# Optimization experiments

Measured on AMD Instinct MI355X. Metric: run time of the kernel, lower is better.

Reference implementation:

```python
import jax, jax.numpy as jnp
import numpy as np

N_BANKS = 16
BAND = 4
D = 32          # n_neurons_per_hidd_bank
N_IN = 3072     # n_input_neurons
N_OUT = 1000    # n_output_neurons
B = 8192        # batch size
IDX_INPUT = [0, 1]
IDX_OUTPUT = [14, 15]
# edge list (source, target), target-major, ascending sources per target --
# matches the torch loop order (np.where over bank_conn[:, i_target])
EDGES = [(s, t) for t in range(N_BANKS) for s in range(max(0, t - BAND), t)]
E = len(EDGES)  # 54
TGT_EDGES = [[e for e, (s, t) in enumerate(EDGES) if t == tt] for tt in range(N_BANKS)]
BN_EPS = 1e-5


def _bn(a):
    # BatchNorm1d in training mode: batch mean, biased batch variance
    m = a.mean(axis=0)
    v = a.var(axis=0)
    return (a - m) * jax.lax.rsqrt(v + BN_EPS)


def setup_inputs() -> dict:
    key = jax.random.key(0)
    ks = jax.random.split(key, 8)
    return {
        "x": jax.random.normal(ks[0], (B, N_IN), jnp.float32),
        "bn_gamma": jnp.ones((N_IN,), jnp.float32),
        "bn_beta": jnp.zeros((N_IN,), jnp.float32),
        "W_in": jax.random.normal(ks[1], (len(IDX_INPUT), N_IN, D), jnp.float32) / np.float32(np.sqrt(N_IN)),
        "b_in": jax.random.normal(ks[2], (len(IDX_INPUT), D), jnp.float32) / np.float32(np.sqrt(N_IN)),
        "Wg": jax.random.normal(ks[3], (E, D), jnp.float32) / np.float32(np.sqrt(D)),
        "Wd": jax.random.normal(ks[4], (E, D, D), jnp.float32) / np.float32(np.sqrt(D)),
        "bd": jax.random.normal(ks[5], (E, D), jnp.float32) / np.float32(np.sqrt(D)),
        "Wout": jax.random.normal(ks[6], (len(IDX_OUTPUT), D, N_OUT), jnp.float32) / np.float32(np.sqrt(D)),
    }


def reference(x, bn_gamma, bn_beta, W_in, b_in, Wg, Wd, bd, Wout):
    # input batch norm (affine)
    x = _bn(x) * bn_gamma + bn_beta
    acts = [None] * N_BANKS
    for k, i in enumerate(IDX_INPUT):
        acts[i] = jax.nn.relu(x @ W_in[k] + b_in[k])  # [B, D]
    total_gate = jnp.zeros((x.shape[0], 1), x.dtype)
    for t in range(N_BANKS):
        acc = acts[t]  # non-None only for input banks
        for e in TGT_EDGES[t]:
            s = EDGES[e][0]
            gate = jnp.clip(acts[s] @ Wg[e], 0.0, 1.0)[:, None]  # hardtanh(.,0,1), [B,1]
            total_gate = total_gate + gate
            data = acts[s] @ Wd[e] + bd[e]                       # [B, D]
            acc = gate * data if acc is None else acc + gate * data
        acts[t] = _bn(jax.nn.relu(acc))  # hidden batch norm, affine=False
    output = None
    for k, i in enumerate(IDX_OUTPUT):
        d = acts[i] @ Wout[k]  # Linear(D, N_OUT, bias=False)
        output = d if output is None else output + d
    return output, total_gate
```

## Files before the change

### kernel.cpp

```cpp
#include <hip/hip_runtime.h>


#define BATCH 8192
#define NIN 3072
#define DD 32
#define NB 16
#define NOUT 1000
#define TGOFF (BATCH * NOUT)
#define BNEPS 1e-5f

#define O_SUM 0
#define O_SUM2 3072
#define O_STATS2 6144
#define O_TG 22528
#define ZERO_FLOATS 30720
#define O_SCALE 30720
#define O_SHIFT 33792
#define O_BIAS 36864
#define O_BP 36928
#define O_ACTS 233536
#define O_ACC (O_ACTS + 2 * BATCH * DD)

__global__ void __launch_bounds__(256) k_stats(const float* __restrict__ x, float* __restrict__ ws) {
    int c = blockIdx.x * 256 + threadIdx.x;
    const float* p = x + (size_t)blockIdx.y * 256 * NIN + c;
    float s = 0.f, s2 = 0.f;
#pragma unroll 8
    for (int i = 0; i < 256; i++) { float v = p[(size_t)i * NIN]; s += v; s2 += v * v; }
    atomicAdd(&ws[O_SUM + c], s);
    atomicAdd(&ws[O_SUM2 + c], s2);
}

__global__ void __launch_bounds__(256) k_prep(float* __restrict__ ws, const float* __restrict__ g,
                                              const float* __restrict__ b, const float* __restrict__ b_in) {
    int c = blockIdx.x * 256 + threadIdx.x;
    float mean = ws[O_SUM + c] * (1.f / BATCH);
    float var = ws[O_SUM2 + c] * (1.f / BATCH) - mean * mean;
    float sc = g[c] * rsqrtf(fmaxf(var, 0.f) + BNEPS);
    ws[O_SCALE + c] = sc;
    ws[O_SHIFT + c] = b[c] - mean * sc;
    if (c < 64) ws[O_BIAS + c] = b_in[c];
}

__global__ void __launch_bounds__(256) k_bias(float* __restrict__ ws, const float* __restrict__ W_in) {
    int bank = blockIdx.x & 1, jc = blockIdx.x >> 1;
    int d = threadIdx.x & 31, js = threadIdx.x >> 5;
    int j0 = jc * 256 + js * 32;
    float a = 0.f;
    for (int j = 0; j < 32; j++)
        a += ws[O_SHIFT + j0 + j] * W_in[(size_t)bank * NIN * DD + (size_t)(j0 + j) * DD + d];
    __shared__ float red[8][32];
    red[js][d] = a;
    __syncthreads();
    if (threadIdx.x < 32) {
        float t = 0.f;
#pragma unroll
        for (int g8 = 0; g8 < 8; g8++) t += red[g8][threadIdx.x];
        atomicAdd(&ws[O_BIAS + bank * 32 + threadIdx.x], t);
    }
}

__global__ void __launch_bounds__(256) k_bfold(float* __restrict__ ws, const float* __restrict__ W_in) {
    int idx = blockIdx.x * 256 + threadIdx.x;
    int j = idx >> 6, c = idx & 63;
    ws[O_BP + idx] = ws[O_SCALE + j] * W_in[(size_t)(c >> 5) * NIN * DD + (size_t)j * DD + (c & 31)];
}

__global__ void __launch_bounds__(256) k_gemm3(const float* __restrict__ x, float* __restrict__ ws) {
    __shared__ float xL[64][20];
    __shared__ float bL[16][64];
    int tid = threadIdx.x;
    int row0 = blockIdx.x * 64;
    int k00 = blockIdx.y * 768;
    const float* bp = ws + O_BP;
    float acc[4][4] = {};
    int tx = tid & 15, rt = tid >> 4;
    int lr = tid >> 2, lq = tid & 3;
    int br = tid >> 4, bq = tid & 15;
    for (int kc = 0; kc < 48; kc++) {
        int k0 = k00 + kc * 16;
        float4 xv = *(const float4*)&x[(size_t)(row0 + lr) * NIN + k0 + lq * 4];
        float4 bv = *(const float4*)&bp[(size_t)(k0 + br) * 64 + bq * 4];
        __syncthreads();
        *(float4*)&xL[lr][lq * 4] = xv;
        *(float4*)&bL[br][bq * 4] = bv;
        __syncthreads();
#pragma unroll
        for (int kk = 0; kk < 16; kk += 4) {
            float4 b0 = *(float4*)&bL[kk][tx * 4];
            float4 b1 = *(float4*)&bL[kk + 1][tx * 4];
            float4 b2 = *(float4*)&bL[kk + 2][tx * 4];
            float4 b3 = *(float4*)&bL[kk + 3][tx * 4];
#pragma unroll
            for (int j = 0; j < 4; j++) {
                float4 xv4 = *(float4*)&xL[rt * 4 + j][kk];
                acc[j][0] += xv4.x * b0.x + xv4.y * b1.x + xv4.z * b2.x + xv4.w * b3.x;
                acc[j][1] += xv4.x * b0.y + xv4.y * b1.y + xv4.z * b2.y + xv4.w * b3.y;
                acc[j][2] += xv4.x * b0.z + xv4.y * b1.z + xv4.z * b2.z + xv4.w * b3.z;
                acc[j][3] += xv4.x * b0.w + xv4.y * b1.w + xv4.z * b2.w + xv4.w * b3.w;
            }
        }
    }
    float* dst = ws + O_ACC + (size_t)blockIdx.y * (BATCH * 64);
#pragma unroll
    for (int j = 0; j < 4; j++) {
        float4 v = make_float4(acc[j][0], acc[j][1], acc[j][2], acc[j][3]);
        *(float4*)&dst[(size_t)(row0 + rt * 4 + j) * 64 + tx * 4] = v;
    }
}

__global__ void __launch_bounds__(256) k_act(float* __restrict__ ws) {
    int i4 = (blockIdx.x * 256 + threadIdx.x) * 4;
    const float* ac = ws + O_ACC;
    float4 s0 = *(const float4*)&ac[i4];
    float4 s1 = *(const float4*)&ac[524288 + i4];
    float4 s2 = *(const float4*)&ac[1048576 + i4];
    float4 s3 = *(const float4*)&ac[1572864 + i4];
    int c = i4 & 63, row = i4 >> 6;
    const float* bias = ws + O_BIAS;
    float4 v;
    v.x = fmaxf(s0.x + s1.x + s2.x + s3.x + bias[c], 0.f);
    v.y = fmaxf(s0.y + s1.y + s2.y + s3.y + bias[c + 1], 0.f);
    v.z = fmaxf(s0.z + s1.z + s2.z + s3.z + bias[c + 2], 0.f);
    v.w = fmaxf(s0.w + s1.w + s2.w + s3.w + bias[c + 3], 0.f);
    int bank = c >> 5, dd = c & 31;
    *(float4*)&ws[O_ACTS + ((size_t)bank * BATCH + row) * DD + dd] = v;
}

__global__ void __launch_bounds__(256) k_bank(int t, float* __restrict__ ws,
                                              const float* __restrict__ Wg, const float* __restrict__ Wd,
                                              const float* __restrict__ bd) {
    __shared__ float asrcL[4][8][32];
    __shared__ float WdL[4][1024];
    __shared__ float mML[4][32], ivL[4][32];
    __shared__ float red[8][64];
    int tid = threadIdx.x;
    int rg = tid >> 5, d = tid & 31;
    int row0 = blockIdx.x * 8;
    int slot = blockIdx.x & 15;
    float* acts = ws + O_ACTS;
    float* stats = ws + O_STATS2;
    int nE = t < 4 ? t : 4;
    int s0 = t - nE;
    int eb = (t <= 4) ? t * (t - 1) / 2 : 10 + 4 * (t - 5);
    for (int p = tid; p < nE * 256; p += 256)
        ((float4*)&WdL[0][0])[p] = ((const float4*)(Wd + (size_t)eb * 1024))[p];
    float wgr[4], bdr[4];
#pragma unroll
    for (int ei = 0; ei < 4; ei++) {
        wgr[ei] = (ei < nE) ? Wg[(eb + ei) * 32 + d] : 0.f;
        bdr[ei] = (ei < nE) ? bd[(eb + ei) * 32 + d] : 0.f;
    }
    if (tid < nE * 32) {
        int si = tid >> 5, dd = tid & 31;
        const float* st = stats + (size_t)(s0 + si) * 16 * 64;
        float sm = 0.f, sq = 0.f;
#pragma unroll
        for (int sl = 0; sl < 16; sl++) { sm += st[sl * 64 + dd]; sq += st[sl * 64 + 32 + dd]; }
        float m = sm * (1.f / BATCH);
        float var = sq * (1.f / BATCH) - m * m;
        mML[si][dd] = m;
        ivL[si][dd] = rsqrtf(fmaxf(var, 0.f) + BNEPS);
    }
    float cur = (t < 2) ? acts[((size_t)t * BATCH + row0 + rg) * DD + d] : 0.f;
    __syncthreads();
#pragma unroll 4
    for (int si = 0; si < nE; si++)
        asrcL[si][rg][d] = (acts[((size_t)(s0 + si) * BATCH + row0 + rg) * DD + d] - mML[si][d]) * ivL[si][d];
    __syncthreads();
    float tg = 0.f;
#pragma unroll
    for (int ei = 0; ei < 4; ei++) {
        if (ei < nE) {
            float g = asrcL[ei][rg][d] * wgr[ei];
            g += __shfl_xor(g, 1); g += __shfl_xor(g, 2); g += __shfl_xor(g, 4);
            g += __shfl_xor(g, 8); g += __shfl_xor(g, 16);
            g = fminf(fmaxf(g, 0.f), 1.f);
            tg += g;
            float dat = bdr[ei];
            const float* ar = asrcL[ei][rg];
            const float* wc = &WdL[ei][d];
#pragma unroll
            for (int k = 0; k < 32; k += 4) {
                float4 a4 = *(const float4*)&ar[k];
                dat += a4.x * wc[k * 32] + a4.y * wc[(k + 1) * 32]
                     + a4.z * wc[(k + 2) * 32] + a4.w * wc[(k + 3) * 32];
            }
            cur += g * dat;
        }
    }
    float v = fmaxf(cur, 0.f);
    acts[((size_t)t * BATCH + row0 + rg) * DD + d] = v;
    if (d == 0 && nE > 0) ws[O_TG + row0 + rg] += tg;
    red[rg][d] = v; red[rg][32 + d] = v * v;
    __syncthreads();
    if (tid < 64) {
        float a = 0.f;
#pragma unroll
        for (int g8 = 0; g8 < 8; g8++) a += red[g8][tid];
        atomicAdd(&stats[((size_t)t * 16 + slot) * 64 + tid], a);
    }
}

__global__ void __launch_bounds__(256) k_out(const float* __restrict__ ws, const float* __restrict__ Wout,
                                             float* __restrict__ out) {
    __shared__ float aLt[32][68];
    __shared__ float wL[32][128];
    __shared__ float mIv[2][2][32];
    int tid = threadIdx.x;
    int row0 = blockIdx.x * 64;
    int col0 = blockIdx.y * 128;
    const float* acts = ws + O_ACTS;
    if (blockIdx.y == 0 && tid < 64) out[TGOFF + row0 + tid] = ws[O_TG + row0 + tid];
    if (tid < 64) {
        int bi = tid >> 5, d = tid & 31;
        const float* st = ws + O_STATS2 + (size_t)(14 + bi) * 16 * 64;
        float sm = 0.f, sq = 0.f;
#pragma unroll
        for (int sl = 0; sl < 16; sl++) { sm += st[sl * 64 + d]; sq += st[sl * 64 + 32 + d]; }
        float m = sm * (1.f / BATCH);
        float var = sq * (1.f / BATCH) - m * m;
        mIv[bi][0][d] = m;
        mIv[bi][1][d] = rsqrtf(fmaxf(var, 0.f) + BNEPS);
    }
    int tx = tid & 31, ty = tid >> 5;
    int c4 = col0 + tx * 4;
    bool c4ok = (c4 + 3 < NOUT);
    float acc[8][4] = {};
    for (int bi = 0; bi < 2; bi++) {
        __syncthreads();
        {
            int d = tid & 31, r0 = tid >> 5;
            float m = mIv[bi][0][d], iv = mIv[bi][1][d];
            const float* ap = acts + ((size_t)(14 + bi) * BATCH + row0) * DD + d;
#pragma unroll
            for (int i = 0; i < 8; i++) {
                int r = r0 + 8 * i;
                aLt[d][r] = (ap[(size_t)r * DD] - m) * iv;
            }
        }
        {
            const float* wp = Wout + (size_t)bi * DD * NOUT + c4;
            int kk0 = tid >> 5;
#pragma unroll
            for (int i = 0; i < 4; i++) {
                int kk = kk0 + 8 * i;
                const float* wr = wp + (size_t)kk * NOUT;
                float4 v;
                if (c4ok) {
                    v = *(const float4*)wr;
                } else {
                    v.x = (c4 + 0 < NOUT) ? wr[0] : 0.f;
                    v.y = (c4 + 1 < NOUT) ? wr[1] : 0.f;
                    v.z = (c4 + 2 < NOUT) ? wr[2] : 0.f;
                    v.w = (c4 + 3 < NOUT) ? wr[3] : 0.f;
                }
                *(float4*)&wL[kk][tx * 4] = v;
            }
        }
        __syncthreads();
#pragma unroll 4
        for (int k = 0; k < 32; k++) {
            float4 w = *(float4*)&wL[k][tx * 4];
            float4 a0 = *(float4*)&aLt[k][ty * 8];
            float4 a1 = *(float4*)&aLt[k][ty * 8 + 4];
            float ar[8] = {a0.x, a0.y, a0.z, a0.w, a1.x, a1.y, a1.z, a1.w};
            float wc[4] = {w.x, w.y, w.z, w.w};
#pragma unroll
            for (int r = 0; r < 8; r++)
#pragma unroll
                for (int c = 0; c < 4; c++)
                    acc[r][c] += ar[r] * wc[c];
        }
    }
    if (c4ok) {
#pragma unroll
        for (int r = 0; r < 8; r++) {
            int row = row0 + ty * 8 + r;
            *(float4*)&out[(size_t)row * NOUT + c4] =
                make_float4(acc[r][0], acc[r][1], acc[r][2], acc[r][3]);
        }
    } else {
#pragma unroll
        for (int r = 0; r < 8; r++) {
            int row = row0 + ty * 8 + r;
#pragma unroll
            for (int c = 0; c < 4; c++)
                if (c4 + c < NOUT) out[(size_t)row * NOUT + c4 + c] = acc[r][c];
        }
    }
}

extern "C" void kernel_launch(void* const* d_in, const int* in_sizes, int n_in,
                              void* d_out, int out_size, void* d_ws, size_t ws_size,
                              hipStream_t stream) {
    (void)in_sizes; (void)n_in; (void)out_size; (void)ws_size;
    const float* x     = (const float*)d_in[0];
    const float* gamma = (const float*)d_in[1];
    const float* beta  = (const float*)d_in[2];
    const float* W_in  = (const float*)d_in[3];
    const float* b_in  = (const float*)d_in[4];
    const float* Wg    = (const float*)d_in[5];
    const float* Wd    = (const float*)d_in[6];
    const float* bd    = (const float*)d_in[7];
    const float* Wout  = (const float*)d_in[8];
    float* out = (float*)d_out;
    float* ws  = (float*)d_ws;

    hipMemsetAsync(d_ws, 0, ZERO_FLOATS * sizeof(float), stream);
    k_stats<<<dim3(12, 32), 256, 0, stream>>>(x, ws);
    k_prep<<<12, 256, 0, stream>>>(ws, gamma, beta, b_in);
    k_bias<<<24, 256, 0, stream>>>(ws, W_in);
    k_bfold<<<768, 256, 0, stream>>>(ws, W_in);
    k_gemm3<<<dim3(128, 4), 256, 0, stream>>>(x, ws);
    k_act<<<512, 256, 0, stream>>>(ws);
    for (int t = 0; t < NB; t++)
        k_bank<<<1024, 256, 0, stream>>>(t, ws, Wg, Wd, bd);
    k_out<<<dim3(128, 8), 256, 0, stream>>>(ws, Wout, out);
}
```

Before: 409.7 us.

## Double-buffer input GEMM, fuse bank-0 stats into k_act, split stats grid

The input GEMM now double-buffers its shared-memory tiles, prefetching the next K chunk into registers while computing the current one, so each iteration needs one barrier instead of two. k_act now also computes the bank-0 batch-norm sum and sum-of-squares and atomically adds them into the stats slots, which lets the bank loop start at t=1 and skip one kernel launch. The stats kernel's grid is doubled along the batch axis, with each block covering half as many rows, to expose more parallelism at the cost of more atomics. The skipped bank-0 launch is only correct if k_bank's t=0 path did nothing beyond those stats, such as normalising bank 0 in place.

Result: slower. 436.0 us (+6.4%).

```diff
diff --git a/kernel.cpp b/kernel.cpp
--- a/kernel.cpp
+++ b/kernel.cpp
@@ -23,10 +23,10 @@
 
 __global__ void __launch_bounds__(256) k_stats(const float* __restrict__ x, float* __restrict__ ws) {
     int c = blockIdx.x * 256 + threadIdx.x;
-    const float* p = x + (size_t)blockIdx.y * 256 * NIN + c;
+    const float* p = x + (size_t)blockIdx.y * 128 * NIN + c;
     float s = 0.f, s2 = 0.f;
 #pragma unroll 8
-    for (int i = 0; i < 256; i++) { float v = p[(size_t)i * NIN]; s += v; s2 += v * v; }
+    for (int i = 0; i < 128; i++) { float v = p[(size_t)i * NIN]; s += v; s2 += v * v; }
     atomicAdd(&ws[O_SUM + c], s);
     atomicAdd(&ws[O_SUM2 + c], s2);
 }
@@ -67,8 +67,8 @@
 }
 
 __global__ void __launch_bounds__(256) k_gemm3(const float* __restrict__ x, float* __restrict__ ws) {
-    __shared__ float xL[64][20];
-    __shared__ float bL[16][64];
+    __shared__ float xL[2][64][20];
+    __shared__ float bL[2][16][64];
     int tid = threadIdx.x;
     int row0 = blockIdx.x * 64;
     int k00 = blockIdx.y * 768;
@@ -77,29 +77,40 @@
     int tx = tid & 15, rt = tid >> 4;
     int lr = tid >> 2, lq = tid & 3;
     int br = tid >> 4, bq = tid & 15;
+    const float* xp = &x[(size_t)(row0 + lr) * NIN + k00 + lq * 4];
+    const float* bpp = &bp[(size_t)(k00 + br) * 64 + bq * 4];
+    float4 xv = *(const float4*)xp;
+    float4 bv = *(const float4*)bpp;
+    *(float4*)&xL[0][lr][lq * 4] = xv;
+    *(float4*)&bL[0][br][bq * 4] = bv;
+    __syncthreads();
+#pragma unroll 2
     for (int kc = 0; kc < 48; kc++) {
-        int k0 = k00 + kc * 16;
-        float4 xv = *(const float4*)&x[(size_t)(row0 + lr) * NIN + k0 + lq * 4];
-        float4 bv = *(const float4*)&bp[(size_t)(k0 + br) * 64 + bq * 4];
-        __syncthreads();
-        *(float4*)&xL[lr][lq * 4] = xv;
-        *(float4*)&bL[br][bq * 4] = bv;
-        __syncthreads();
+        int cur = kc & 1;
+        if (kc < 47) {
+            xv = *(const float4*)(xp + (kc + 1) * 16);
+            bv = *(const float4*)(bpp + (size_t)(kc + 1) * 1024);
+        }
 #pragma unroll
         for (int kk = 0; kk < 16; kk += 4) {
-            float4 b0 = *(float4*)&bL[kk][tx * 4];
-            float4 b1 = *(float4*)&bL[kk + 1][tx * 4];
-            float4 b2 = *(float4*)&bL[kk + 2][tx * 4];
-            float4 b3 = *(float4*)&bL[kk + 3][tx * 4];
+            float4 b0 = *(float4*)&bL[cur][kk][tx * 4];
+            float4 b1 = *(float4*)&bL[cur][kk + 1][tx * 4];
+            float4 b2 = *(float4*)&bL[cur][kk + 2][tx * 4];
+            float4 b3 = *(float4*)&bL[cur][kk + 3][tx * 4];
 #pragma unroll
             for (int j = 0; j < 4; j++) {
-                float4 xv4 = *(float4*)&xL[rt * 4 + j][kk];
+                float4 xv4 = *(float4*)&xL[cur][rt * 4 + j][kk];
                 acc[j][0] += xv4.x * b0.x + xv4.y * b1.x + xv4.z * b2.x + xv4.w * b3.x;
                 acc[j][1] += xv4.x * b0.y + xv4.y * b1.y + xv4.z * b2.y + xv4.w * b3.y;
                 acc[j][2] += xv4.x * b0.z + xv4.y * b1.z + xv4.z * b2.z + xv4.w * b3.z;
                 acc[j][3] += xv4.x * b0.w + xv4.y * b1.w + xv4.z * b2.w + xv4.w * b3.w;
             }
         }
+        if (kc < 47) {
+            *(float4*)&xL[cur ^ 1][lr][lq * 4] = xv;
+            *(float4*)&bL[cur ^ 1][br][bq * 4] = bv;
+        }
+        __syncthreads();
     }
     float* dst = ws + O_ACC + (size_t)blockIdx.y * (BATCH * 64);
 #pragma unroll
@@ -110,7 +121,10 @@
 }
 
 __global__ void __launch_bounds__(256) k_act(float* __restrict__ ws) {
-    int i4 = (blockIdx.x * 256 + threadIdx.x) * 4;
+    __shared__ float sred[16][32];
+    __shared__ float qred[16][32];
+    int tid = threadIdx.x;
+    int i4 = (blockIdx.x * 256 + tid) * 4;
     const float* ac = ws + O_ACC;
     float4 s0 = *(const float4*)&ac[i4];
     float4 s1 = *(const float4*)&ac[524288 + i4];
@@ -125,6 +139,21 @@
     v.w = fmaxf(s0.w + s1.w + s2.w + s3.w + bias[c + 3], 0.f);
     int bank = c >> 5, dd = c & 31;
     *(float4*)&ws[O_ACTS + ((size_t)bank * BATCH + row) * DD + dd] = v;
+    int r16 = tid >> 4;
+    if (bank == 0) {
+        *(float4*)&sred[r16][dd] = v;
+        *(float4*)&qred[r16][dd] = make_float4(v.x * v.x, v.y * v.y, v.z * v.z, v.w * v.w);
+    }
+    __syncthreads();
+    if (tid < 32) {
+        float sm = 0.f, sq = 0.f;
+#pragma unroll
+        for (int r = 0; r < 16; r++) { sm += sred[r][tid]; sq += qred[r][tid]; }
+        int slot = blockIdx.x & 15;
+        float* st = ws + O_STATS2 + (size_t)slot * 64;
+        atomicAdd(&st[tid], sm);
+        atomicAdd(&st[32 + tid], sq);
+    }
 }
 
 __global__ void __launch_bounds__(256) k_bank(int t, float* __restrict__ ws,
@@ -308,13 +337,13 @@
     float* ws  = (float*)d_ws;
 
     hipMemsetAsync(d_ws, 0, ZERO_FLOATS * sizeof(float), stream);
-    k_stats<<<dim3(12, 32), 256, 0, stream>>>(x, ws);
+    k_stats<<<dim3(12, 64), 256, 0, stream>>>(x, ws);
     k_prep<<<12, 256, 0, stream>>>(ws, gamma, beta, b_in);
     k_bias<<<24, 256, 0, stream>>>(ws, W_in);
     k_bfold<<<768, 256, 0, stream>>>(ws, W_in);
     k_gemm3<<<dim3(128, 4), 256, 0, stream>>>(x, ws);
     k_act<<<512, 256, 0, stream>>>(ws);
-    for (int t = 0; t < NB; t++)
+    for (int t = 1; t < NB; t++)
         k_bank<<<1024, 256, 0, stream>>>(t, ws, Wg, Wd, bd);
     k_out<<<dim3(128, 8), 256, 0, stream>>>(ws, Wout, out);
 }
```
